# Performance work log

Measured on AMD Instinct MI355X. Metric: run time of the kernel, lower is better.

## Reference

```python
import jax, jax.numpy as jnp
import numpy as np

DIM = 1024
NUM_HEADS = 16
HEAD_DIM = DIM // NUM_HEADS
INNER_ITR = 4
INNER_LR = 1.0
SCALE_QKV = 1.0


def setup_inputs() -> dict:
    key = jax.random.key(0)
    k1, k2, k3 = jax.random.split(key, 3)
    B, N, C = 8, 1024, DIM
    x = jax.random.normal(k1, (B, N, C), dtype=jnp.float32)
    # Xavier-uniform-ish scaled dense kernels
    w_qkv = jax.random.normal(k2, (C, 3 * C), dtype=jnp.float32) * (1.0 / np.sqrt(C))
    w_proj = jax.random.normal(k3, (C, C), dtype=jnp.float32) * (1.0 / np.sqrt(C))
    b_proj = jnp.zeros((C,), dtype=jnp.float32)
    return {"x": x, "w_qkv": w_qkv, "w_proj": w_proj, "b_proj": b_proj, "training": 0}


def _mttt_base(q, k, v):
    """MTTT 'base' inner loop: per (B,H) linear model W,b trained by
    INNER_ITR full-batch GD steps on MSE reconstruction of v from k,
    then applied to q. Shapes: q,k,v are (B, H, N, d)."""
    B, H, N, d = q.shape
    W = jnp.zeros((B, H, d, d), dtype=q.dtype)
    b = jnp.zeros((B, H, 1, d), dtype=q.dtype)
    invN = 1.0 / N
    for _ in range(INNER_ITR):  # small fixed iteration count
        pred = jnp.einsum('bhnd,bhde->bhne', k, W) + b   # (B,H,N,d)
        err = pred - v
        gW = jnp.einsum('bhnd,bhne->bhde', k, err) * invN
        gb = jnp.mean(err, axis=2, keepdims=True)
        W = W - INNER_LR * gW
        b = b - INNER_LR * gb
    return jnp.einsum('bhnd,bhde->bhne', q, W) + b       # (B,H,N,d)


def reference(x, w_qkv, w_proj, b_proj, training):
    B, N, C = x.shape
    H, d = NUM_HEADS, HEAD_DIM
    qkv = jnp.einsum('bnc,ce->bne', x, w_qkv)            # (B,N,3C), qkv_bias=False
    qkv = qkv.reshape(B, N, 3, H, d).transpose(2, 0, 3, 1, 4)  # (3,B,H,N,d)
    qkv = qkv * SCALE_QKV
    q, k, v = qkv[0], qkv[1], qkv[2]
    # qk_norm=False -> identity; scale_q=False -> no q scaling
    out = _mttt_base(q, k, v)                            # (B,H,N,d)
    out = out.transpose(0, 2, 1, 3).reshape(B, N, C)
    out = jnp.einsum('bnc,cd->bnd', out, w_proj) + b_proj
    # proj dropout deterministic (training=False)
    return out
```

## Files before the change

kernel.cpp:

```cpp
#include <hip/hip_runtime.h>


#define SEQ    1024
#define NBATCH 8
#define DIMC   1024
#define NHEAD  16
#define HDIM   64
#define MROWS  8192
#define NQKV   3072
#define KDS    136

typedef __attribute__((ext_vector_type(8))) __bf16 bf16x8;
typedef __attribute__((ext_vector_type(4))) float  f32x4;

__device__ __forceinline__ unsigned short f2b(float f) {
  union { float f; unsigned int u; } v; v.f = f;
  unsigned int r = (v.u + 0x7FFFu + ((v.u >> 16) & 1u)) >> 16;
  return (unsigned short)r;
}
__device__ __forceinline__ float b2f(unsigned short u) {
  union { unsigned int u; float f; } v; v.u = ((unsigned int)u) << 16;
  return v.f;
}

__device__ __forceinline__ void load_lds16(const void* g, void* l) {
  __builtin_amdgcn_global_load_lds(
      (__attribute__((address_space(1))) void*)(void*)(g),
      (__attribute__((address_space(3))) void*)(l), 16, 0, 0);
}

#define FENCE asm volatile("" ::: "memory")
#define BAR   __builtin_amdgcn_s_barrier()

__global__ __launch_bounds__(256) void prep(const float* __restrict__ x,
                                            const float* __restrict__ wq,
                                            const float* __restrict__ wp,
                                            unsigned short* __restrict__ xb,
                                            unsigned short* __restrict__ wqT,
                                            unsigned short* __restrict__ wpT) {
  __shared__ unsigned short tile[32][33];
  const int bid = blockIdx.x, tid = threadIdx.x;
  if (bid < 8192) {
    int i = bid * 256 + tid;
    float4 v = ((const float4*)x)[i];
    ushort4 o;
    o.x = f2b(v.x); o.y = f2b(v.y); o.z = f2b(v.z); o.w = f2b(v.w);
    ((ushort4*)xb)[i] = o;
    return;
  }
  const float* in; unsigned short* out; int R, Cc, tix;
  if (bid < 8192 + 3072) { tix = bid - 8192; in = wq; out = wqT; R = 1024; Cc = 3072; }
  else                   { tix = bid - 8192 - 3072; in = wp; out = wpT; R = 1024; Cc = 1024; }
  const int nbx = Cc / 32;
  const int c0 = (tix % nbx) * 32, r0 = (tix / nbx) * 32;
  const int tx = tid & 31, ty = tid >> 5;
  for (int i = ty; i < 32; i += 8)
    tile[i][tx] = f2b(in[(size_t)(r0 + i) * Cc + c0 + tx]);
  __syncthreads();
  for (int i = ty; i < 32; i += 8)
    out[(size_t)(c0 + i) * R + r0 + tx] = tile[tx][i];
}

template <int BM, int BN, int WM, int WN, int ASTRIDE, int BMODE, int PERB>
__device__ __forceinline__
void gemm_r3(const unsigned short* __restrict__ A,
             const unsigned short* __restrict__ BT,
             void* __restrict__ Cout,
             const float* __restrict__ bias,
             int N, int NBN) {
  constexpr int THREADS = WM * WN * 64;
  constexpr int TR      = THREADS / 4;
  constexpr int ABYTES  = BM * 64;
  constexpr int TBYTES  = (BM + BN) * 64;
  constexpr int CALLS   = TBYTES / (THREADS * 16);
  constexpr int NT      = 32;

  extern __shared__ __align__(16) char ldsb[];

  const int tid  = threadIdx.x;
  const int lane = tid & 63, wave = tid >> 6;
  const int wr = wave / WN, wc = wave % WN;
  const int frow = lane & 15, g4 = lane >> 4;
  const int cz = (g4 ^ ((frow >> 1) & 3)) * 16;

  const int cpx = gridDim.x >> 3;
  const int wg  = (blockIdx.x & 7) * cpx + (blockIdx.x >> 3);
  const int bm = wg / NBN, bn = wg % NBN;
  const size_t m0 = (size_t)bm * BM, n0 = (size_t)bn * BN;

  const unsigned short* BTb = PERB ? (BT + (m0 >> 10) * (size_t)(1024 * 1024)) : BT;

  const int trow = tid >> 2;
  const int scol = ((tid & 3) ^ ((tid >> 3) & 3)) * 8;
  const unsigned short* psrc[CALLS];
#pragma unroll
  for (int c = 0; c < CALLS; ++c) {
    const int rr = c * TR + trow;
    psrc[c] = (rr < BM) ? (A + (m0 + rr) * (size_t)ASTRIDE + scol)
                        : (BTb + (size_t)(n0 + rr - BM) * 1024 + scol);
  }

  f32x4 acc[4][4];
  if (BMODE == 2) {
    const float* bp = bias + (m0 >> 10) * (size_t)N;
#pragma unroll
    for (int j = 0; j < 4; ++j) {
      float4 bv = *(const float4*)&bp[n0 + wc * 64 + j * 16 + g4 * 4];
      f32x4 t; t[0] = bv.x; t[1] = bv.y; t[2] = bv.z; t[3] = bv.w;
#pragma unroll
      for (int i = 0; i < 4; ++i) acc[i][j] = t;
    }
  } else {
#pragma unroll
    for (int i = 0; i < 4; ++i)
#pragma unroll
      for (int j = 0; j < 4; ++j) acc[i][j] = f32x4{0.f, 0.f, 0.f, 0.f};
  }

  auto stage = [&](int tk, int buf) {
    char* base = ldsb + buf * TBYTES + wave * 1024;
#pragma unroll
    for (int c = 0; c < CALLS; ++c)
      load_lds16(psrc[c] + tk * 32, base + c * (THREADS * 16));
  };

  const int aoff = (wr * 64 + frow) * 64 + cz;
  const int boff = ABYTES + (wc * 64 + frow) * 64 + cz;

  stage(0, 0); stage(1, 1);
  asm volatile("s_waitcnt vmcnt(%0)" :: "i"(CALLS) : "memory");
  FENCE; BAR;

  int bcur = 0, bpre = 2;
#pragma unroll 1
  for (int t = 0; t < NT; ++t) {
    if (t + 2 < NT) stage(t + 2, bpre);
    const char* rb = ldsb + bcur * TBYTES;
    bf16x8 af[4], bq[4];
#pragma unroll
    for (int i = 0; i < 4; ++i) af[i] = *(const bf16x8*)(rb + aoff + i * 1024);
#pragma unroll
    for (int j = 0; j < 4; ++j) bq[j] = *(const bf16x8*)(rb + boff + j * 1024);
#pragma unroll
    for (int i = 0; i < 4; ++i)
#pragma unroll
      for (int j = 0; j < 4; ++j)
        acc[i][j] = __builtin_amdgcn_mfma_f32_16x16x32_bf16(bq[j], af[i],
                                                            acc[i][j], 0, 0, 0);
    if (t + 2 < NT) asm volatile("s_waitcnt vmcnt(%0)" :: "i"(CALLS) : "memory");
    else            asm volatile("s_waitcnt vmcnt(0)" ::: "memory");
    FENCE; BAR;
    bcur = (bcur == 2) ? 0 : bcur + 1;
    bpre = (bpre == 2) ? 0 : bpre + 1;
  }

  const size_t mbase = m0 + wr * 64 + frow;
  const size_t nbase = n0 + wc * 64 + g4 * 4;
  if (BMODE == 2) {
    float* C = (float*)Cout;
#pragma unroll
    for (int i = 0; i < 4; ++i)
#pragma unroll
      for (int j = 0; j < 4; ++j) {
        float4 o; o.x = acc[i][j][0]; o.y = acc[i][j][1];
        o.z = acc[i][j][2]; o.w = acc[i][j][3];
        *(float4*)&C[(mbase + i * 16) * N + nbase + j * 16] = o;
      }
  } else {
    unsigned short* C = (unsigned short*)Cout;
#pragma unroll
    for (int i = 0; i < 4; ++i)
#pragma unroll
      for (int j = 0; j < 4; ++j) {
        ushort4 o; o.x = f2b(acc[i][j][0]); o.y = f2b(acc[i][j][1]);
        o.z = f2b(acc[i][j][2]); o.w = f2b(acc[i][j][3]);
        *(ushort4*)&C[(mbase + i * 16) * N + nbase + j * 16] = o;
      }
  }
}

__global__ __launch_bounds__(512, 4) void g_qkv(const unsigned short* __restrict__ A,
                                                const unsigned short* __restrict__ BT,
                                                void* __restrict__ C,
                                                const float* __restrict__ bias, int N, int NBN) {
  gemm_r3<128, 256, 2, 4, 1024, 0, 0>(A, BT, C, bias, N, NBN);
}
__global__ __launch_bounds__(256, 4) void g_out(const unsigned short* __restrict__ A,
                                                const unsigned short* __restrict__ BT,
                                                void* __restrict__ C,
                                                const float* __restrict__ bias, int N, int NBN) {
  gemm_r3<64, 256, 1, 4, NQKV, 2, 1>(A, BT, C, bias, N, NBN);
}

__global__ __launch_bounds__(256) void stats_gd(const unsigned short* __restrict__ qkvb,
                                                unsigned short* __restrict__ Wfb,
                                                float* __restrict__ bvec) {
  __shared__ float Gs[64][68];
  __shared__ float Ps[64][68];
  __shared__ float Ws[64][68];
  __shared__ unsigned short kd[64][KDS];
  __shared__ unsigned short vd[64][KDS];
  __shared__ float mks[64], mvs[64], bs[64];

  const int bh = blockIdx.x, b = bh >> 4, h = bh & 15;
  const int tid = threadIdx.x;
  const int lane = tid & 63, wave = tid >> 6;
  const int frow = lane & 15;
  const int fk = (lane >> 4) * 8;

  const unsigned short* kg = qkvb + (size_t)b * 1024 * 3072 + 1024 + h * 64;
  const unsigned short* vg = qkvb + (size_t)b * 1024 * 3072 + 2048 + h * 64;

  typedef __attribute__((ext_vector_type(8))) unsigned short u16x8;
  u16x8 onesu = {0x3F80, 0x3F80, 0x3F80, 0x3F80, 0x3F80, 0x3F80, 0x3F80, 0x3F80};
  const bf16x8 ones = __builtin_bit_cast(bf16x8, onesu);

  f32x4 accG[4], accP[4], accK1, accV1;
#pragma unroll
  for (int j = 0; j < 4; ++j) {
    accG[j] = f32x4{0.f, 0.f, 0.f, 0.f};
    accP[j] = f32x4{0.f, 0.f, 0.f, 0.f};
  }
  accK1 = f32x4{0.f, 0.f, 0.f, 0.f};
  accV1 = f32x4{0.f, 0.f, 0.f, 0.f};

  const int sd = tid & 63;
  const int ng = tid >> 6;

  for (int ch = 0; ch < 8; ++ch) {
    __syncthreads();
    const int nb0 = ch * 128 + ng * 32;
#pragma unroll
    for (int s = 0; s < 4; ++s) {
      alignas(16) unsigned short tk[8], tv[8];
#pragma unroll
      for (int t = 0; t < 8; ++t) {
        tk[t] = kg[(size_t)(nb0 + s * 8 + t) * 3072 + sd];
        tv[t] = vg[(size_t)(nb0 + s * 8 + t) * 3072 + sd];
      }
      *(uint4*)&kd[sd][ng * 32 + s * 8] = *(const uint4*)tk;
      *(uint4*)&vd[sd][ng * 32 + s * 8] = *(const uint4*)tv;
    }
    __syncthreads();
#pragma unroll
    for (int ks = 0; ks < 4; ++ks) {
      const int nb = ks * 32 + fk;
      bf16x8 afk = *(const bf16x8*)&kd[wave * 16 + frow][nb];
      bf16x8 afv = *(const bf16x8*)&vd[wave * 16 + frow][nb];
      bf16x8 kf[4], vf[4];
#pragma unroll
      for (int j = 0; j < 4; ++j) {
        kf[j] = *(const bf16x8*)&kd[j * 16 + frow][nb];
        vf[j] = *(const bf16x8*)&vd[j * 16 + frow][nb];
      }
#pragma unroll
      for (int j = 0; j < 4; ++j) {
        accG[j] = __builtin_amdgcn_mfma_f32_16x16x32_bf16(afk, kf[j], accG[j], 0, 0, 0);
        accP[j] = __builtin_amdgcn_mfma_f32_16x16x32_bf16(afk, vf[j], accP[j], 0, 0, 0);
      }
      accK1 = __builtin_amdgcn_mfma_f32_16x16x32_bf16(afk, ones, accK1, 0, 0, 0);
      accV1 = __builtin_amdgcn_mfma_f32_16x16x32_bf16(afv, ones, accV1, 0, 0, 0);
    }
  }

  const float invN = 1.0f / (float)SEQ;
  const int orow = wave * 16 + (lane >> 4) * 4;
#pragma unroll
  for (int j = 0; j < 4; ++j)
#pragma unroll
    for (int r = 0; r < 4; ++r) {
      Gs[orow + r][j * 16 + frow] = accG[j][r] * invN;
      Ps[orow + r][j * 16 + frow] = accP[j][r] * invN;
    }
  if (frow == 0) {
#pragma unroll
    for (int r = 0; r < 4; ++r) {
      mks[orow + r] = accK1[r] * invN;
      mvs[orow + r] = accV1[r] * invN;
    }
  }
  const int r = tid >> 2;
  const int c0 = (tid & 3) * 16;
  if (tid < 64) bs[tid] = 0.f;
#pragma unroll
  for (int c = 0; c < 16; ++c) Ws[r][c0 + c] = 0.f;
  __syncthreads();

  for (int it = 0; it < 4; ++it) {
    float wn[16];
#pragma unroll
    for (int c = 0; c < 16; ++c)
      wn[c] = Ws[r][c0 + c] + Ps[r][c0 + c] - mks[r] * bs[c0 + c];
    for (int j = 0; j < 64; ++j) {
      float g = Gs[r][j];
#pragma unroll
      for (int c = 0; c < 16; ++c) wn[c] -= g * Ws[j][c0 + c];
    }
    float bn = 0.f;
    if (tid < 64) {
      bn = mvs[tid];
      for (int j = 0; j < 64; ++j) bn -= mks[j] * Ws[j][tid];
    }
    __syncthreads();
#pragma unroll
    for (int c = 0; c < 16; ++c) Ws[r][c0 + c] = wn[c];
    if (tid < 64) bs[tid] = bn;
    __syncthreads();
  }

  unsigned short* wout = Wfb + (size_t)bh * HDIM * HDIM;
#pragma unroll
  for (int c = 0; c < 16; ++c)
    wout[(size_t)r * HDIM + c0 + c] = f2b(Ws[r][c0 + c]);
  if (tid < 64) bvec[(size_t)bh * HDIM + tid] = bs[tid];
}

__global__ __launch_bounds__(256) void wc_build(const unsigned short* __restrict__ wpT,
                                                const unsigned short* __restrict__ Wfb,
                                                unsigned short* __restrict__ WcT,
                                                const float* __restrict__ wp,
                                                const float* __restrict__ bvec,
                                                float* __restrict__ part) {
  const int tid = threadIdx.x;
  if (blockIdx.y == 4) {
    if (blockIdx.x >= 64) return;
    const int p  = (blockIdx.x & 3) * 256 + tid;
    const int cc = blockIdx.x >> 2;
    float s[8];
#pragma unroll
    for (int b = 0; b < 8; ++b) s[b] = 0.f;
    const int c0 = cc * 64;
    for (int c = c0; c < c0 + 64; ++c) {
      float w = wp[(size_t)c * 1024 + p];
#pragma unroll
      for (int b = 0; b < 8; ++b) s[b] += bvec[b * 1024 + c] * w;
    }
    float* dst = part + (size_t)cc * 8192;
#pragma unroll
    for (int b = 0; b < 8; ++b) dst[b * 1024 + p] = s[b];
    return;
  }
  const int bh = blockIdx.x;
  const int pblk = blockIdx.y;
  const int b = bh >> 4, h = bh & 15;
  const int lane = tid & 63, wave = tid >> 6;
  const int frow = lane & 15, g4 = lane >> 4, fk = g4 * 8;
  const int p0 = pblk * 256 + wave * 64;

  f32x4 acc[4][4];
#pragma unroll
  for (int i = 0; i < 4; ++i)
#pragma unroll
    for (int j = 0; j < 4; ++j) acc[i][j] = f32x4{0.f, 0.f, 0.f, 0.f};

  const unsigned short* wb = Wfb + (size_t)bh * 4096;
#pragma unroll
  for (int kk = 0; kk < 2; ++kk) {
    bf16x8 af[4], bq[4];
#pragma unroll
    for (int i = 0; i < 4; ++i)
      af[i] = *(const bf16x8*)&wpT[(size_t)(p0 + i * 16 + frow) * 1024 + h * 64 + kk * 32 + fk];
#pragma unroll
    for (int j = 0; j < 4; ++j)
      bq[j] = *(const bf16x8*)&wb[(size_t)(j * 16 + frow) * 64 + kk * 32 + fk];
#pragma unroll
    for (int i = 0; i < 4; ++i)
#pragma unroll
      for (int j = 0; j < 4; ++j)
        acc[i][j] = __builtin_amdgcn_mfma_f32_16x16x32_bf16(bq[j], af[i], acc[i][j], 0, 0, 0);
  }

  unsigned short* dst = WcT + (size_t)b * 1024 * 1024;
#pragma unroll
  for (int i = 0; i < 4; ++i)
#pragma unroll
    for (int j = 0; j < 4; ++j) {
      ushort4 o; o.x = f2b(acc[i][j][0]); o.y = f2b(acc[i][j][1]);
      o.z = f2b(acc[i][j][2]); o.w = f2b(acc[i][j][3]);
      *(ushort4*)&dst[(size_t)(p0 + i * 16 + frow) * 1024 + h * 64 + j * 16 + g4 * 4] = o;
    }
}

__global__ __launch_bounds__(256) void bc_reduce(const float* __restrict__ part,
                                                 const float* __restrict__ b_proj,
                                                 float* __restrict__ bc) {
  const int idx = blockIdx.x * 256 + threadIdx.x;
  const int p = idx & 1023;
  float s = b_proj[p];
#pragma unroll
  for (int cc = 0; cc < 16; ++cc) s += part[(size_t)cc * 8192 + idx];
  bc[idx] = s;
}

extern "C" void kernel_launch(void* const* d_in, const int* in_sizes, int n_in,
                              void* d_out, int out_size, void* d_ws, size_t ws_size,
                              hipStream_t stream) {
  const float* x      = (const float*)d_in[0];
  const float* w_qkv  = (const float*)d_in[1];
  const float* w_proj = (const float*)d_in[2];
  const float* b_proj = (const float*)d_in[3];

  char* ws = (char*)d_ws;
  unsigned short* xb    = (unsigned short*)(ws + 0);
  unsigned short* wqT   = (unsigned short*)(ws + 16777216);
  unsigned short* wpT   = (unsigned short*)(ws + 23068672);
  unsigned short* qkvb  = (unsigned short*)(ws + 25165824);
  unsigned short* WcT   = (unsigned short*)(ws + 109051904);
  unsigned short* Wfb   = (unsigned short*)(ws + 125829120);
  float*          bvec  = (float*)(ws + 126877696);
  float*          bc    = (float*)(ws + 126910464);
  float*          bpart = (float*)(ws + 126943232);
  if (ws_size < (size_t)127467520) return;

  hipFuncSetAttribute((const void*)g_qkv, hipFuncAttributeMaxDynamicSharedMemorySize, 73728);
  hipFuncSetAttribute((const void*)g_out, hipFuncAttributeMaxDynamicSharedMemorySize, 61440);

  prep<<<dim3(8192 + 3072 + 1024), 256, 0, stream>>>(x, w_qkv, w_proj, xb, wqT, wpT);
  g_qkv<<<dim3(768), dim3(512), 73728, stream>>>(xb, wqT, qkvb, nullptr, NQKV, 12);
  stats_gd<<<128, 256, 0, stream>>>(qkvb, Wfb, bvec);
  wc_build<<<dim3(128, 5), 256, 0, stream>>>(wpT, Wfb, WcT, w_proj, bvec, bpart);
  bc_reduce<<<32, 256, 0, stream>>>(bpart, b_proj, bc);
  g_out<<<dim3(512), dim3(256), 61440, stream>>>(qkvb, WcT, d_out, bc, DIMC, 4);
}
```

Before: 166.8 us.

## Widen QKV GEMM warp tiles and stage K/V via async LDS loads in stats kernel

The QKV GEMM template is generalized so each wave computes a configurable number of MFMA fragments. The QKV launch moves from 8 waves to 4 waves per 128x256 tile, so each wave now handles 4x8 fragments, which raises register use but improves reuse of LDS fragments. The stats_gd kernel replaces strided scalar 2-byte global gathers with 16-byte global_load_lds copies into a row-major staging buffer, then transposes in LDS. It also overlays the float G/P/W buffers on the K/V staging area to reduce LDS footprint, at the cost of smaller chunks and more barriers.

```diff
diff --git a/kernel.cpp b/kernel.cpp
--- a/kernel.cpp
+++ b/kernel.cpp
@@ -8,7 +8,6 @@
 #define HDIM   64
 #define MROWS  8192
 #define NQKV   3072
-#define KDS    136
 
 typedef __attribute__((ext_vector_type(8))) __bf16 bf16x8;
 typedef __attribute__((ext_vector_type(4))) float  f32x4;
@@ -17,10 +16,6 @@
   union { float f; unsigned int u; } v; v.f = f;
   unsigned int r = (v.u + 0x7FFFu + ((v.u >> 16) & 1u)) >> 16;
   return (unsigned short)r;
-}
-__device__ __forceinline__ float b2f(unsigned short u) {
-  union { unsigned int u; float f; } v; v.u = ((unsigned int)u) << 16;
-  return v.f;
 }
 
 __device__ __forceinline__ void load_lds16(const void* g, void* l) {
@@ -69,6 +64,8 @@
              const float* __restrict__ bias,
              int N, int NBN) {
   constexpr int THREADS = WM * WN * 64;
+  constexpr int MF      = BM / (WM * 16);
+  constexpr int NF      = BN / (WN * 16);
   constexpr int TR      = THREADS / 4;
   constexpr int ABYTES  = BM * 64;
   constexpr int TBYTES  = (BM + BN) * 64;
@@ -100,21 +97,21 @@
                         : (BTb + (size_t)(n0 + rr - BM) * 1024 + scol);
   }
 
-  f32x4 acc[4][4];
+  f32x4 acc[MF][NF];
   if (BMODE == 2) {
     const float* bp = bias + (m0 >> 10) * (size_t)N;
 #pragma unroll
-    for (int j = 0; j < 4; ++j) {
-      float4 bv = *(const float4*)&bp[n0 + wc * 64 + j * 16 + g4 * 4];
+    for (int j = 0; j < NF; ++j) {
+      float4 bv = *(const float4*)&bp[n0 + wc * (BN / WN) + j * 16 + g4 * 4];
       f32x4 t; t[0] = bv.x; t[1] = bv.y; t[2] = bv.z; t[3] = bv.w;
 #pragma unroll
-      for (int i = 0; i < 4; ++i) acc[i][j] = t;
+      for (int i = 0; i < MF; ++i) acc[i][j] = t;
     }
   } else {
 #pragma unroll
-    for (int i = 0; i < 4; ++i)
-#pragma unroll
-      for (int j = 0; j < 4; ++j) acc[i][j] = f32x4{0.f, 0.f, 0.f, 0.f};
+    for (int i = 0; i < MF; ++i)
+#pragma unroll
+      for (int j = 0; j < NF; ++j) acc[i][j] = f32x4{0.f, 0.f, 0.f, 0.f};
   }
 
   auto stage = [&](int tk, int buf) {
@@ -124,8 +121,8 @@
       load_lds16(psrc[c] + tk * 32, base + c * (THREADS * 16));
   };
 
-  const int aoff = (wr * 64 + frow) * 64 + cz;
-  const int boff = ABYTES + (wc * 64 + frow) * 64 + cz;
+  const int aoff = (wr * (BM / WM) + frow) * 64 + cz;
+  const int boff = ABYTES + (wc * (BN / WN) + frow) * 64 + cz;
 
   stage(0, 0); stage(1, 1);
   asm volatile("s_waitcnt vmcnt(%0)" :: "i"(CALLS) : "memory");
@@ -136,15 +133,15 @@
   for (int t = 0; t < NT; ++t) {
     if (t + 2 < NT) stage(t + 2, bpre);
     const char* rb = ldsb + bcur * TBYTES;
-    bf16x8 af[4], bq[4];
-#pragma unroll
-    for (int i = 0; i < 4; ++i) af[i] = *(const bf16x8*)(rb + aoff + i * 1024);
-#pragma unroll
-    for (int j = 0; j < 4; ++j) bq[j] = *(const bf16x8*)(rb + boff + j * 1024);
-#pragma unroll
-    for (int i = 0; i < 4; ++i)
-#pragma unroll
-      for (int j = 0; j < 4; ++j)
+    bf16x8 af[MF], bq[NF];
+#pragma unroll
+    for (int i = 0; i < MF; ++i) af[i] = *(const bf16x8*)(rb + aoff + i * 1024);
+#pragma unroll
+    for (int j = 0; j < NF; ++j) bq[j] = *(const bf16x8*)(rb + boff + j * 1024);
+#pragma unroll
+    for (int i = 0; i < MF; ++i)
+#pragma unroll
+      for (int j = 0; j < NF; ++j)
         acc[i][j] = __builtin_amdgcn_mfma_f32_16x16x32_bf16(bq[j], af[i],
                                                             acc[i][j], 0, 0, 0);
     if (t + 2 < NT) asm volatile("s_waitcnt vmcnt(%0)" :: "i"(CALLS) : "memory");
@@ -154,14 +151,14 @@
     bpre = (bpre == 2) ? 0 : bpre + 1;
   }
 
-  const size_t mbase = m0 + wr * 64 + frow;
-  const size_t nbase = n0 + wc * 64 + g4 * 4;
+  const size_t mbase = m0 + wr * (BM / WM) + frow;
+  const size_t nbase = n0 + wc * (BN / WN) + g4 * 4;
   if (BMODE == 2) {
     float* C = (float*)Cout;
 #pragma unroll
-    for (int i = 0; i < 4; ++i)
-#pragma unroll
-      for (int j = 0; j < 4; ++j) {
+    for (int i = 0; i < MF; ++i)
+#pragma unroll
+      for (int j = 0; j < NF; ++j) {
         float4 o; o.x = acc[i][j][0]; o.y = acc[i][j][1];
         o.z = acc[i][j][2]; o.w = acc[i][j][3];
         *(float4*)&C[(mbase + i * 16) * N + nbase + j * 16] = o;
@@ -169,9 +166,9 @@
   } else {
     unsigned short* C = (unsigned short*)Cout;
 #pragma unroll
-    for (int i = 0; i < 4; ++i)
-#pragma unroll
-      for (int j = 0; j < 4; ++j) {
+    for (int i = 0; i < MF; ++i)
+#pragma unroll
+      for (int j = 0; j < NF; ++j) {
         ushort4 o; o.x = f2b(acc[i][j][0]); o.y = f2b(acc[i][j][1]);
         o.z = f2b(acc[i][j][2]); o.w = f2b(acc[i][j][3]);
         *(ushort4*)&C[(mbase + i * 16) * N + nbase + j * 16] = o;
@@ -179,11 +176,11 @@
   }
 }
 
-__global__ __launch_bounds__(512, 4) void g_qkv(const unsigned short* __restrict__ A,
+__global__ __launch_bounds__(256, 2) void g_qkv(const unsigned short* __restrict__ A,
                                                 const unsigned short* __restrict__ BT,
                                                 void* __restrict__ C,
                                                 const float* __restrict__ bias, int N, int NBN) {
-  gemm_r3<128, 256, 2, 4, 1024, 0, 0>(A, BT, C, bias, N, NBN);
+  gemm_r3<128, 256, 2, 2, 1024, 0, 0>(A, BT, C, bias, N, NBN);
 }
 __global__ __launch_bounds__(256, 4) void g_out(const unsigned short* __restrict__ A,
                                                 const unsigned short* __restrict__ BT,
@@ -195,11 +192,14 @@
 __global__ __launch_bounds__(256) void stats_gd(const unsigned short* __restrict__ qkvb,
                                                 unsigned short* __restrict__ Wfb,
                                                 float* __restrict__ bvec) {
-  __shared__ float Gs[64][68];
-  __shared__ float Ps[64][68];
-  __shared__ float Ws[64][68];
-  __shared__ unsigned short kd[64][KDS];
-  __shared__ unsigned short vd[64][KDS];
+  __shared__ __align__(16) char smem[52224];
+  unsigned short (*kd)[136] = (unsigned short(*)[136])(smem);
+  unsigned short (*vd)[136] = (unsigned short(*)[136])(smem + 17408);
+  unsigned short (*kn)[64]  = (unsigned short(*)[64])(smem + 34816);
+  unsigned short (*vn)[64]  = (unsigned short(*)[64])(smem + 43008);
+  float (*Gs)[68] = (float(*)[68])(smem);
+  float (*Ps)[68] = (float(*)[68])(smem + 17408);
+  float (*Ws)[68] = (float(*)[68])(smem + 34816);
   __shared__ float mks[64], mvs[64], bs[64];
 
   const int bh = blockIdx.x, b = bh >> 4, h = bh & 15;
@@ -224,26 +224,33 @@
   accK1 = f32x4{0.f, 0.f, 0.f, 0.f};
   accV1 = f32x4{0.f, 0.f, 0.f, 0.f};
 
-  const int sd = tid & 63;
-  const int ng = tid >> 6;
-
-  for (int ch = 0; ch < 8; ++ch) {
-    __syncthreads();
-    const int nb0 = ch * 128 + ng * 32;
-#pragma unroll
-    for (int s = 0; s < 4; ++s) {
-      alignas(16) unsigned short tk[8], tv[8];
-#pragma unroll
-      for (int t = 0; t < 8; ++t) {
-        tk[t] = kg[(size_t)(nb0 + s * 8 + t) * 3072 + sd];
-        tv[t] = vg[(size_t)(nb0 + s * 8 + t) * 3072 + sd];
+  const size_t srcn = (size_t)(tid >> 3) * 3072 + (tid & 7) * 8;
+  const int td = tid & 63, tng = tid >> 6;
+
+  for (int ch = 0; ch < 16; ++ch) {
+    const size_t nb0 = (size_t)ch * 64;
+#pragma unroll
+    for (int c = 0; c < 2; ++c) {
+      load_lds16(kg + (nb0 + 32 * c) * 3072 + srcn, (char*)kn + c * 4096 + wave * 1024);
+      load_lds16(vg + (nb0 + 32 * c) * 3072 + srcn, (char*)vn + c * 4096 + wave * 1024);
+    }
+    asm volatile("s_waitcnt vmcnt(0)" ::: "memory");
+    FENCE; BAR;
+    {
+      alignas(16) unsigned short pk[16], pv[16];
+#pragma unroll
+      for (int j = 0; j < 16; ++j) {
+        pk[j] = kn[tng * 16 + j][td];
+        pv[j] = vn[tng * 16 + j][td];
       }
-      *(uint4*)&kd[sd][ng * 32 + s * 8] = *(const uint4*)tk;
-      *(uint4*)&vd[sd][ng * 32 + s * 8] = *(const uint4*)tv;
-    }
-    __syncthreads();
-#pragma unroll
-    for (int ks = 0; ks < 4; ++ks) {
+      *(uint4*)&kd[td][tng * 16]     = *(const uint4*)pk;
+      *(uint4*)&kd[td][tng * 16 + 8] = *(const uint4*)(pk + 8);
+      *(uint4*)&vd[td][tng * 16]     = *(const uint4*)pv;
+      *(uint4*)&vd[td][tng * 16 + 8] = *(const uint4*)(pv + 8);
+    }
+    FENCE; BAR;
+#pragma unroll
+    for (int ks = 0; ks < 2; ++ks) {
       const int nb = ks * 32 + fk;
       bf16x8 afk = *(const bf16x8*)&kd[wave * 16 + frow][nb];
       bf16x8 afv = *(const bf16x8*)&vd[wave * 16 + frow][nb];
@@ -261,6 +268,7 @@
       accK1 = __builtin_amdgcn_mfma_f32_16x16x32_bf16(afk, ones, accK1, 0, 0, 0);
       accV1 = __builtin_amdgcn_mfma_f32_16x16x32_bf16(afv, ones, accV1, 0, 0, 0);
     }
+    FENCE; BAR;
   }
 
   const float invN = 1.0f / (float)SEQ;
@@ -416,7 +424,7 @@
   hipFuncSetAttribute((const void*)g_out, hipFuncAttributeMaxDynamicSharedMemorySize, 61440);
 
   prep<<<dim3(8192 + 3072 + 1024), 256, 0, stream>>>(x, w_qkv, w_proj, xb, wqT, wpT);
-  g_qkv<<<dim3(768), dim3(512), 73728, stream>>>(xb, wqT, qkvb, nullptr, NQKV, 12);
+  g_qkv<<<dim3(768), dim3(256), 73728, stream>>>(xb, wqT, qkvb, nullptr, NQKV, 12);
   stats_gd<<<128, 256, 0, stream>>>(qkvb, Wfb, bvec);
   wc_build<<<dim3(128, 5), 256, 0, stream>>>(wpT, Wfb, WcT, w_proj, bvec, bpart);
   bc_reduce<<<32, 256, 0, stream>>>(bpart, b_proj, bc);
```

Result: no change. 168.7 us (+1.2%).
